# Kernel tuning notes

Hardware: AMD Instinct MI355X
Metric: run time of the kernel (lower is better)

The kernel has to match this reference:

```python
import jax, jax.numpy as jnp
import numpy as np

ALPHA = 1.8   # Levy stability index (undefined global in source; chosen heavy-tailed)
BETA = 0.0    # symmetric
SIGMA = 0.5
DEPTH = 25
DIM = 64
HID = 100
BATCH = 262144


def _levy_noise(u_raw, w_raw):
    """Chambers-Mallows-Stuck sampler for symmetric alpha-stable (beta=0).
    u_raw, w_raw ~ U(0,1); returns clipped noise, scale=0.1, clamp [-10,10]."""
    U = jnp.pi * (u_raw - 0.5)                       # U(-pi/2, pi/2)
    W = -jnp.log(jnp.clip(w_raw, 1e-12, 1.0))        # Exp(1)
    inv_a = 1.0 / ALPHA
    X = (jnp.sin(ALPHA * U) / jnp.cos(U) ** inv_a) * \
        (jnp.cos(U - ALPHA * U) / jnp.clip(W, 1e-12, None)) ** ((1.0 - ALPHA) * inv_a)
    return jnp.clip(0.1 * X, -10.0, 10.0)


def setup_inputs() -> dict:
    key = jax.random.key(0)
    ks = jax.random.split(key, 8)
    d, h = DIM, HID
    return {
        "x": jax.random.normal(ks[0], (BATCH, d), dtype=jnp.float32),
        "u_raw": jax.random.uniform(ks[1], (DEPTH, d), dtype=jnp.float32),
        "w_raw": jax.random.uniform(ks[2], (DEPTH, d), dtype=jnp.float32),
        "W_down": jax.random.normal(ks[3], (d, d), dtype=jnp.float32) / np.sqrt(d),
        "b_down": jnp.zeros((d,), jnp.float32),
        "W_drift": jax.random.normal(ks[4], (d, d), dtype=jnp.float32) / np.sqrt(d),
        "b_drift": jnp.zeros((d,), jnp.float32),
        "W1": jax.random.normal(ks[5], (d, h), dtype=jnp.float32) / np.sqrt(d),
        "b1": jnp.zeros((h,), jnp.float32),
        "W2": jax.random.normal(ks[6], (h, 1), dtype=jnp.float32) / np.sqrt(h),
        "b2": jnp.zeros((1,), jnp.float32),
    }


def reference(x, u_raw, w_raw, W_down, b_down, W_drift, b_drift, W1, b1, W2, b2):
    dt = 1.0 / DEPTH
    out = x @ W_down + b_down                                   # [B, d]
    # diffusion logit on the INITIAL state, held fixed through the loop
    logit = jax.nn.relu(out @ W1 + b1) @ W2 + b2                # [B, 1]
    scale = SIGMA * jax.nn.sigmoid(logit) * dt ** (1.0 / ALPHA)  # [B, 1]
    noise = _levy_noise(u_raw, w_raw)                           # [DEPTH, d]

    def step(out, n):
        drift = jax.nn.relu(out @ W_drift + b_drift) + out      # DriftNet: relu(lin)+x
        return out + drift * dt + scale * n, None

    out, _ = jax.lax.scan(step, out, noise)
    drift_out = jax.nn.relu(out @ W_drift + b_drift) + out
    return drift_out, out
```

## Files before the change

kernel.cpp:

```cpp
#include <hip/hip_runtime.h>
#include <hip/hip_bf16.h>

#define DEPTH 25
#define DIM   64
#define HID   100

typedef _Float16 f16x4 __attribute__((ext_vector_type(4)));
typedef float    f32x4 __attribute__((ext_vector_type(4)));
typedef float    f32x2 __attribute__((ext_vector_type(2)));

__global__ __launch_bounds__(64) void levy_noise_kernel(
    const float* __restrict__ u_raw, const float* __restrict__ w_raw,
    float* __restrict__ noise)
{
    const int idx = blockIdx.x * 64 + threadIdx.x;
    if (idx >= DEPTH * DIM) return;
    float u = u_raw[idx];
    float w = w_raw[idx];
    float U  = 3.14159265358979323846f * (u - 0.5f);
    float Wv = -logf(fminf(fmaxf(w, 1e-12f), 1.0f));
    float t1 = sinf(1.8f * U) / powf(cosf(U), 0.5555555555555556f);
    float ratio = cosf(0.8f * U) / fmaxf(Wv, 1e-12f);
    float X = t1 * powf(ratio, -0.4444444444444444f);
    noise[idx] = fminf(fmaxf(0.1f * X, -10.0f), 10.0f);
}

__global__ __launch_bounds__(256) void sdenet_fused(
    const float* __restrict__ x,      const float* __restrict__ noise_g,
    const float* __restrict__ W_down, const float* __restrict__ b_down,
    const float* __restrict__ W_drift,const float* __restrict__ b_drift,
    const float* __restrict__ W1,     const float* __restrict__ b1,
    const float* __restrict__ W2,     const float* __restrict__ b2,
    float* __restrict__ out, int batch)
{
    __shared__ float noise_lds[DEPTH * DIM];

    const int tid = threadIdx.x;
    {
        const float4* src = (const float4*)noise_g;
        float4* dst = (float4*)noise_lds;
        for (int idx = tid; idx < DEPTH * DIM / 4; idx += 256)
            dst[idx] = src[idx];
    }
    __syncthreads();

    const int wave = tid >> 6;
    const int lane = tid & 63;
    const int r    = lane & 15;
    const int g    = lane >> 4;
    const int row  = blockIdx.x * 64 + wave * 16 + r;
    const float dt = 0.04f;

    f16x4 bfrag[4];
    #pragma unroll
    for (int kt = 0; kt < 4; ++kt) {
        const float4 xv = *(const float4*)(x + row * DIM + kt * 16 + g * 4);
        f16x4 t;
        t[0] = (_Float16)xv.x; t[1] = (_Float16)xv.y;
        t[2] = (_Float16)xv.z; t[3] = (_Float16)xv.w;
        bfrag[kt] = t;
    }

    f32x2 out2[4][2];
    #pragma unroll
    for (int Mt = 0; Mt < 4; ++Mt) {
        f32x4 acc = *(const f32x4*)(b_down + Mt * 16 + g * 4);
        #pragma unroll
        for (int kt = 0; kt < 4; ++kt) {
            f16x4 a;
            #pragma unroll
            for (int i = 0; i < 4; ++i)
                a[i] = (_Float16)W_down[(kt * 16 + g * 4 + i) * DIM + Mt * 16 + r];
            acc = __builtin_amdgcn_mfma_f32_16x16x16f16(a, bfrag[kt], acc, 0, 0, 0);
        }
        out2[Mt][0][0] = acc[0]; out2[Mt][0][1] = acc[1];
        out2[Mt][1][0] = acc[2]; out2[Mt][1][1] = acc[3];
    }

    #pragma unroll
    for (int kt = 0; kt < 4; ++kt) {
        f16x4 t;
        t[0] = (_Float16)out2[kt][0][0]; t[1] = (_Float16)out2[kt][0][1];
        t[2] = (_Float16)out2[kt][1][0]; t[3] = (_Float16)out2[kt][1][1];
        bfrag[kt] = t;
    }

    float partial = 0.0f;
    #pragma unroll
    for (int Mt = 0; Mt < 7; ++Mt) {
        f32x4 acc;
        #pragma unroll
        for (int reg = 0; reg < 4; ++reg) {
            int n = Mt * 16 + g * 4 + reg;
            acc[reg] = (n < HID) ? b1[n] : 0.0f;
        }
        const int ncol = Mt * 16 + r;
        #pragma unroll
        for (int kt = 0; kt < 4; ++kt) {
            f16x4 a;
            #pragma unroll
            for (int i = 0; i < 4; ++i) {
                int k = kt * 16 + g * 4 + i;
                float v = (ncol < HID) ? W1[k * HID + ncol] : 0.0f;
                a[i] = (_Float16)v;
            }
            acc = __builtin_amdgcn_mfma_f32_16x16x16f16(a, bfrag[kt], acc, 0, 0, 0);
        }
        #pragma unroll
        for (int reg = 0; reg < 4; ++reg) {
            int n = Mt * 16 + g * 4 + reg;
            if (n < HID) partial += fmaxf(acc[reg], 0.0f) * W2[n];
        }
    }
    partial += __shfl_xor(partial, 16);
    partial += __shfl_xor(partial, 32);
    const float logit = partial + b2[0];
    const float scale = 0.5f * (1.0f / (1.0f + expf(-logit)))
                      * powf(0.04f, 1.0f / 1.8f);
    const f32x2 scale2 = { scale, scale };
    const f32x2 c104   = { 1.04f, 1.04f };
    const f32x2 zero2  = { 0.0f, 0.0f };

    f16x4 aWd[4][4];
    #pragma unroll
    for (int Mt = 0; Mt < 4; ++Mt)
        #pragma unroll
        for (int kt = 0; kt < 4; ++kt) {
            f16x4 a;
            #pragma unroll
            for (int i = 0; i < 4; ++i)
                a[i] = (_Float16)(dt * W_drift[(kt * 16 + g * 4 + i) * DIM + Mt * 16 + r]);
            aWd[Mt][kt] = a;
        }
    f32x4 biasd[4];
    #pragma unroll
    for (int Mt = 0; Mt < 4; ++Mt) {
        f32x4 b = *(const f32x4*)(b_drift + Mt * 16 + g * 4);
        biasd[Mt][0] = b[0] * dt; biasd[Mt][1] = b[1] * dt;
        biasd[Mt][2] = b[2] * dt; biasd[Mt][3] = b[3] * dt;
    }

    for (int t = 0; t < DEPTH; ++t) {
        f32x4 nz[4];
        #pragma unroll
        for (int Mt = 0; Mt < 4; ++Mt)
            nz[Mt] = *(const f32x4*)(noise_lds + t * DIM + Mt * 16 + g * 4);

        f32x4 acc[4];
        #pragma unroll
        for (int Mt = 0; Mt < 4; ++Mt) {
            acc[Mt] = biasd[Mt];
            #pragma unroll
            for (int kt = 0; kt < 4; ++kt)
                acc[Mt] = __builtin_amdgcn_mfma_f32_16x16x16f16(aWd[Mt][kt], bfrag[kt], acc[Mt], 0, 0, 0);
        }
        #pragma unroll
        for (int Mt = 0; Mt < 4; ++Mt) {
            #pragma unroll
            for (int h = 0; h < 2; ++h) {
                f32x2 a2 = { acc[Mt][2 * h], acc[Mt][2 * h + 1] };
                f32x2 n2 = { nz[Mt][2 * h],  nz[Mt][2 * h + 1] };
                f32x2 rel = __builtin_elementwise_max(a2, zero2);
                f32x2 tmp = __builtin_elementwise_fma(out2[Mt][h], c104, rel);
                out2[Mt][h] = __builtin_elementwise_fma(scale2, n2, tmp);
            }
        }
        #pragma unroll
        for (int kt = 0; kt < 4; ++kt) {
            f16x4 tt;
            tt[0] = (_Float16)out2[kt][0][0]; tt[1] = (_Float16)out2[kt][0][1];
            tt[2] = (_Float16)out2[kt][1][0]; tt[3] = (_Float16)out2[kt][1][1];
            bfrag[kt] = tt;
        }
    }

    const long long out2_off = (long long)batch * DIM;
    #pragma unroll
    for (int Mt = 0; Mt < 4; ++Mt) {
        f32x4 acc = biasd[Mt];
        #pragma unroll
        for (int kt = 0; kt < 4; ++kt)
            acc = __builtin_amdgcn_mfma_f32_16x16x16f16(aWd[Mt][kt], bfrag[kt], acc, 0, 0, 0);
        float o0 = out2[Mt][0][0], o1 = out2[Mt][0][1];
        float o2 = out2[Mt][1][0], o3 = out2[Mt][1][1];
        float4 dv, ov;
        dv.x = fmaf(fmaxf(acc[0], 0.0f), 25.0f, o0);
        dv.y = fmaf(fmaxf(acc[1], 0.0f), 25.0f, o1);
        dv.z = fmaf(fmaxf(acc[2], 0.0f), 25.0f, o2);
        dv.w = fmaf(fmaxf(acc[3], 0.0f), 25.0f, o3);
        ov.x = o0; ov.y = o1; ov.z = o2; ov.w = o3;
        *(float4*)(out + (long long)row * DIM + Mt * 16 + g * 4) = dv;
        *(float4*)(out + out2_off + (long long)row * DIM + Mt * 16 + g * 4) = ov;
    }
}

extern "C" void kernel_launch(void* const* d_in, const int* in_sizes, int n_in,
                              void* d_out, int out_size, void* d_ws, size_t ws_size,
                              hipStream_t stream) {
    const float* x       = (const float*)d_in[0];
    const float* u_raw   = (const float*)d_in[1];
    const float* w_raw   = (const float*)d_in[2];
    const float* W_down  = (const float*)d_in[3];
    const float* b_down  = (const float*)d_in[4];
    const float* W_drift = (const float*)d_in[5];
    const float* b_drift = (const float*)d_in[6];
    const float* W1      = (const float*)d_in[7];
    const float* b1      = (const float*)d_in[8];
    const float* W2      = (const float*)d_in[9];
    const float* b2      = (const float*)d_in[10];
    float* out   = (float*)d_out;
    float* noise = (float*)d_ws;

    const int batch = in_sizes[0] / DIM;
    const int blocks = batch / 64;

    levy_noise_kernel<<<DEPTH, 64, 0, stream>>>(u_raw, w_raw, noise);
    sdenet_fused<<<blocks, 256, 0, stream>>>(
        x, noise, W_down, b_down, W_drift, b_drift,
        W1, b1, W2, b2, out, batch);
}
```

Measured before the change: 280.0 us.

## Prepack weight fragments in prep kernel and process two row groups per wave

A single-block prep kernel now computes the Levy noise and also pre-converts W_down, dt-scaled W_drift and padded W1 into per-lane fp16 MFMA fragment order in device globals. The main kernel loads these with vector loads instead of doing strided scalar gathers and conversions. Each wave now handles two 16-row groups (128 rows per block), so the weight fragments are reused and two independent MFMA chains can interleave. Register pressure roughly doubles for state and accumulators, which may reduce occupancy, and the single-block prep kernel runs serially before the main kernel.

```diff
diff --git a/kernel.cpp b/kernel.cpp
--- a/kernel.cpp
+++ b/kernel.cpp
@@ -6,38 +6,74 @@
 #define HID   100
 
 typedef _Float16 f16x4 __attribute__((ext_vector_type(4)));
+typedef _Float16 f16x2 __attribute__((ext_vector_type(2)));
 typedef float    f32x4 __attribute__((ext_vector_type(4)));
 typedef float    f32x2 __attribute__((ext_vector_type(2)));
 
-__global__ __launch_bounds__(64) void levy_noise_kernel(
+static __device__ __forceinline__ f16x2 cvt_pk(float a, float b) {
+    return __builtin_bit_cast(f16x2, __builtin_amdgcn_cvt_pkrtz(a, b));
+}
+
+__device__ __align__(16) float    g_noise[DEPTH * DIM];
+__device__ __align__(16) float    g_b1p[112];
+__device__ __align__(16) float    g_W2p[112];
+__device__ __align__(16) _Float16 g_frWdown [64 * 64];
+__device__ __align__(16) _Float16 g_frWdrift[64 * 64];
+__device__ __align__(16) _Float16 g_frW1    [64 * 112];
+
+__global__ __launch_bounds__(256) void prep_kernel(
     const float* __restrict__ u_raw, const float* __restrict__ w_raw,
-    float* __restrict__ noise)
+    const float* __restrict__ W_down, const float* __restrict__ W_drift,
+    const float* __restrict__ W1,     const float* __restrict__ b1,
+    const float* __restrict__ W2)
 {
-    const int idx = blockIdx.x * 64 + threadIdx.x;
-    if (idx >= DEPTH * DIM) return;
-    float u = u_raw[idx];
-    float w = w_raw[idx];
-    float U  = 3.14159265358979323846f * (u - 0.5f);
-    float Wv = -logf(fminf(fmaxf(w, 1e-12f), 1.0f));
-    float t1 = sinf(1.8f * U) / powf(cosf(U), 0.5555555555555556f);
-    float ratio = cosf(0.8f * U) / fmaxf(Wv, 1e-12f);
-    float X = t1 * powf(ratio, -0.4444444444444444f);
-    noise[idx] = fminf(fmaxf(0.1f * X, -10.0f), 10.0f);
+    const int tid = threadIdx.x;
+
+    for (int idx = tid; idx < DEPTH * DIM; idx += 256) {
+        float u = u_raw[idx];
+        float w = w_raw[idx];
+        float U  = 3.14159265358979323846f * (u - 0.5f);
+        float Wv = -logf(fminf(fmaxf(w, 1e-12f), 1.0f));
+        float t1 = sinf(1.8f * U) / powf(cosf(U), 0.5555555555555556f);
+        float ratio = cosf(0.8f * U) / fmaxf(Wv, 1e-12f);
+        float X = t1 * powf(ratio, -0.4444444444444444f);
+        g_noise[idx] = fminf(fmaxf(0.1f * X, -10.0f), 10.0f);
+    }
+    if (tid < 112) {
+        g_b1p[tid] = (tid < HID) ? b1[tid] : 0.0f;
+        g_W2p[tid] = (tid < HID) ? W2[tid] : 0.0f;
+    }
+    if (tid < 64) {
+        const int l = tid, r = l & 15, g = l >> 4;
+        for (int Mt = 0; Mt < 4; ++Mt)
+            for (int kt = 0; kt < 4; ++kt)
+                for (int i = 0; i < 4; ++i) {
+                    int k = kt * 16 + g * 4 + i, col = Mt * 16 + r;
+                    g_frWdown [l * 64 + Mt * 16 + kt * 4 + i] = (_Float16)W_down[k * DIM + col];
+                    g_frWdrift[l * 64 + Mt * 16 + kt * 4 + i] = (_Float16)(0.04f * W_drift[k * DIM + col]);
+                }
+        for (int Mt = 0; Mt < 7; ++Mt) {
+            int ncol = Mt * 16 + r;
+            for (int kt = 0; kt < 4; ++kt)
+                for (int i = 0; i < 4; ++i) {
+                    int k = kt * 16 + g * 4 + i;
+                    g_frW1[l * 112 + Mt * 16 + kt * 4 + i] =
+                        (ncol < HID) ? (_Float16)W1[k * HID + ncol] : (_Float16)0.0f;
+                }
+        }
+    }
 }
 
 __global__ __launch_bounds__(256) void sdenet_fused(
-    const float* __restrict__ x,      const float* __restrict__ noise_g,
-    const float* __restrict__ W_down, const float* __restrict__ b_down,
-    const float* __restrict__ W_drift,const float* __restrict__ b_drift,
-    const float* __restrict__ W1,     const float* __restrict__ b1,
-    const float* __restrict__ W2,     const float* __restrict__ b2,
-    float* __restrict__ out, int batch)
+    const float* __restrict__ x,
+    const float* __restrict__ b_down, const float* __restrict__ b_drift,
+    const float* __restrict__ b2, float* __restrict__ out, int batch)
 {
     __shared__ float noise_lds[DEPTH * DIM];
 
     const int tid = threadIdx.x;
     {
-        const float4* src = (const float4*)noise_g;
+        const float4* src = (const float4*)g_noise;
         float4* dst = (float4*)noise_lds;
         for (int idx = tid; idx < DEPTH * DIM / 4; idx += 256)
             dst[idx] = src[idx];
@@ -48,97 +84,90 @@
     const int lane = tid & 63;
     const int r    = lane & 15;
     const int g    = lane >> 4;
-    const int row  = blockIdx.x * 64 + wave * 16 + r;
-    const float dt = 0.04f;
-
-    f16x4 bfrag[4];
+    const int row0 = blockIdx.x * 128 + wave * 32 + r;
+    const int row1 = row0 + 16;
+
+    f16x4 bfrag[2][4];
     #pragma unroll
     for (int kt = 0; kt < 4; ++kt) {
-        const float4 xv = *(const float4*)(x + row * DIM + kt * 16 + g * 4);
-        f16x4 t;
-        t[0] = (_Float16)xv.x; t[1] = (_Float16)xv.y;
-        t[2] = (_Float16)xv.z; t[3] = (_Float16)xv.w;
-        bfrag[kt] = t;
-    }
-
-    f32x2 out2[4][2];
+        const float4 xv0 = *(const float4*)(x + (long long)row0 * DIM + kt * 16 + g * 4);
+        const float4 xv1 = *(const float4*)(x + (long long)row1 * DIM + kt * 16 + g * 4);
+        f16x2 a0 = cvt_pk(xv0.x, xv0.y), a1 = cvt_pk(xv0.z, xv0.w);
+        f16x2 b0 = cvt_pk(xv1.x, xv1.y), b1v = cvt_pk(xv1.z, xv1.w);
+        bfrag[0][kt] = (f16x4){a0[0], a0[1], a1[0], a1[1]};
+        bfrag[1][kt] = (f16x4){b0[0], b0[1], b1v[0], b1v[1]};
+    }
+
+    f32x2 st[2][4][2];
     #pragma unroll
     for (int Mt = 0; Mt < 4; ++Mt) {
-        f32x4 acc = *(const f32x4*)(b_down + Mt * 16 + g * 4);
+        const f32x4 bdn = *(const f32x4*)(b_down + Mt * 16 + g * 4);
+        #pragma unroll
+        for (int gr = 0; gr < 2; ++gr) {
+            f32x4 acc = bdn;
+            #pragma unroll
+            for (int kt = 0; kt < 4; ++kt) {
+                const f16x4 a = *(const f16x4*)(g_frWdown + lane * 64 + Mt * 16 + kt * 4);
+                acc = __builtin_amdgcn_mfma_f32_16x16x16f16(a, bfrag[gr][kt], acc, 0, 0, 0);
+            }
+            st[gr][Mt][0] = (f32x2){acc[0], acc[1]};
+            st[gr][Mt][1] = (f32x2){acc[2], acc[3]};
+        }
+    }
+    #pragma unroll
+    for (int gr = 0; gr < 2; ++gr)
         #pragma unroll
         for (int kt = 0; kt < 4; ++kt) {
-            f16x4 a;
-            #pragma unroll
-            for (int i = 0; i < 4; ++i)
-                a[i] = (_Float16)W_down[(kt * 16 + g * 4 + i) * DIM + Mt * 16 + r];
-            acc = __builtin_amdgcn_mfma_f32_16x16x16f16(a, bfrag[kt], acc, 0, 0, 0);
-        }
-        out2[Mt][0][0] = acc[0]; out2[Mt][0][1] = acc[1];
-        out2[Mt][1][0] = acc[2]; out2[Mt][1][1] = acc[3];
-    }
-
-    #pragma unroll
-    for (int kt = 0; kt < 4; ++kt) {
-        f16x4 t;
-        t[0] = (_Float16)out2[kt][0][0]; t[1] = (_Float16)out2[kt][0][1];
-        t[2] = (_Float16)out2[kt][1][0]; t[3] = (_Float16)out2[kt][1][1];
-        bfrag[kt] = t;
-    }
-
-    float partial = 0.0f;
+            f16x2 lo = cvt_pk(st[gr][kt][0][0], st[gr][kt][0][1]);
+            f16x2 hi = cvt_pk(st[gr][kt][1][0], st[gr][kt][1][1]);
+            bfrag[gr][kt] = (f16x4){lo[0], lo[1], hi[0], hi[1]};
+        }
+
+    float partial[2] = {0.0f, 0.0f};
     #pragma unroll
     for (int Mt = 0; Mt < 7; ++Mt) {
-        f32x4 acc;
-        #pragma unroll
-        for (int reg = 0; reg < 4; ++reg) {
-            int n = Mt * 16 + g * 4 + reg;
-            acc[reg] = (n < HID) ? b1[n] : 0.0f;
-        }
-        const int ncol = Mt * 16 + r;
-        #pragma unroll
-        for (int kt = 0; kt < 4; ++kt) {
-            f16x4 a;
-            #pragma unroll
-            for (int i = 0; i < 4; ++i) {
-                int k = kt * 16 + g * 4 + i;
-                float v = (ncol < HID) ? W1[k * HID + ncol] : 0.0f;
-                a[i] = (_Float16)v;
-            }
-            acc = __builtin_amdgcn_mfma_f32_16x16x16f16(a, bfrag[kt], acc, 0, 0, 0);
-        }
-        #pragma unroll
-        for (int reg = 0; reg < 4; ++reg) {
-            int n = Mt * 16 + g * 4 + reg;
-            if (n < HID) partial += fmaxf(acc[reg], 0.0f) * W2[n];
-        }
-    }
-    partial += __shfl_xor(partial, 16);
-    partial += __shfl_xor(partial, 32);
-    const float logit = partial + b2[0];
-    const float scale = 0.5f * (1.0f / (1.0f + expf(-logit)))
+        const f32x4 binit = *(const f32x4*)(g_b1p + Mt * 16 + g * 4);
+        const f32x4 w2v   = *(const f32x4*)(g_W2p + Mt * 16 + g * 4);
+        #pragma unroll
+        for (int gr = 0; gr < 2; ++gr) {
+            f32x4 acc = binit;
+            #pragma unroll
+            for (int kt = 0; kt < 4; ++kt) {
+                const f16x4 a = *(const f16x4*)(g_frW1 + lane * 112 + Mt * 16 + kt * 4);
+                acc = __builtin_amdgcn_mfma_f32_16x16x16f16(a, bfrag[gr][kt], acc, 0, 0, 0);
+            }
+            #pragma unroll
+            for (int reg = 0; reg < 4; ++reg)
+                partial[gr] += fmaxf(acc[reg], 0.0f) * w2v[reg];
+        }
+    }
+    f32x2 scl[2];
+    #pragma unroll
+    for (int gr = 0; gr < 2; ++gr) {
+        float p = partial[gr];
+        p += __shfl_xor(p, 16);
+        p += __shfl_xor(p, 32);
+        const float logit = p + b2[0];
+        const float s = 0.5f * (1.0f / (1.0f + expf(-logit)))
                       * powf(0.04f, 1.0f / 1.8f);
-    const f32x2 scale2 = { scale, scale };
-    const f32x2 c104   = { 1.04f, 1.04f };
-    const f32x2 zero2  = { 0.0f, 0.0f };
+        scl[gr] = (f32x2){s, s};
+    }
 
     f16x4 aWd[4][4];
     #pragma unroll
     for (int Mt = 0; Mt < 4; ++Mt)
         #pragma unroll
-        for (int kt = 0; kt < 4; ++kt) {
-            f16x4 a;
-            #pragma unroll
-            for (int i = 0; i < 4; ++i)
-                a[i] = (_Float16)(dt * W_drift[(kt * 16 + g * 4 + i) * DIM + Mt * 16 + r]);
-            aWd[Mt][kt] = a;
-        }
+        for (int kt = 0; kt < 4; ++kt)
+            aWd[Mt][kt] = *(const f16x4*)(g_frWdrift + lane * 64 + Mt * 16 + kt * 4);
     f32x4 biasd[4];
     #pragma unroll
     for (int Mt = 0; Mt < 4; ++Mt) {
         f32x4 b = *(const f32x4*)(b_drift + Mt * 16 + g * 4);
-        biasd[Mt][0] = b[0] * dt; biasd[Mt][1] = b[1] * dt;
-        biasd[Mt][2] = b[2] * dt; biasd[Mt][3] = b[3] * dt;
-    }
+        biasd[Mt] = (f32x4){b[0] * 0.04f, b[1] * 0.04f, b[2] * 0.04f, b[3] * 0.04f};
+    }
+
+    const f32x2 c104 = {1.04f, 1.04f};
+    const f32x2 zero2 = {0.0f, 0.0f};
 
     for (int t = 0; t < DEPTH; ++t) {
         f32x4 nz[4];
@@ -146,51 +175,60 @@
         for (int Mt = 0; Mt < 4; ++Mt)
             nz[Mt] = *(const f32x4*)(noise_lds + t * DIM + Mt * 16 + g * 4);
 
-        f32x4 acc[4];
+        f32x4 acc[2][4];
+        #pragma unroll
+        for (int gr = 0; gr < 2; ++gr)
+            #pragma unroll
+            for (int Mt = 0; Mt < 4; ++Mt) {
+                acc[gr][Mt] = biasd[Mt];
+                #pragma unroll
+                for (int kt = 0; kt < 4; ++kt)
+                    acc[gr][Mt] = __builtin_amdgcn_mfma_f32_16x16x16f16(
+                        aWd[Mt][kt], bfrag[gr][kt], acc[gr][Mt], 0, 0, 0);
+            }
+        #pragma unroll
+        for (int gr = 0; gr < 2; ++gr) {
+            #pragma unroll
+            for (int Mt = 0; Mt < 4; ++Mt) {
+                #pragma unroll
+                for (int h = 0; h < 2; ++h) {
+                    f32x2 a2 = {acc[gr][Mt][2 * h], acc[gr][Mt][2 * h + 1]};
+                    f32x2 n2 = {nz[Mt][2 * h], nz[Mt][2 * h + 1]};
+                    f32x2 rel = __builtin_elementwise_max(a2, zero2);
+                    f32x2 tmp = __builtin_elementwise_fma(st[gr][Mt][h], c104, rel);
+                    st[gr][Mt][h] = __builtin_elementwise_fma(scl[gr], n2, tmp);
+                }
+            }
+            #pragma unroll
+            for (int kt = 0; kt < 4; ++kt) {
+                f16x2 lo = cvt_pk(st[gr][kt][0][0], st[gr][kt][0][1]);
+                f16x2 hi = cvt_pk(st[gr][kt][1][0], st[gr][kt][1][1]);
+                bfrag[gr][kt] = (f16x4){lo[0], lo[1], hi[0], hi[1]};
+            }
+        }
+    }
+
+    const long long out2_off = (long long)batch * DIM;
+    #pragma unroll
+    for (int gr = 0; gr < 2; ++gr) {
+        const long long rowg = (gr == 0) ? row0 : row1;
         #pragma unroll
         for (int Mt = 0; Mt < 4; ++Mt) {
-            acc[Mt] = biasd[Mt];
+            f32x4 acc = biasd[Mt];
             #pragma unroll
             for (int kt = 0; kt < 4; ++kt)
-                acc[Mt] = __builtin_amdgcn_mfma_f32_16x16x16f16(aWd[Mt][kt], bfrag[kt], acc[Mt], 0, 0, 0);
-        }
-        #pragma unroll
-        for (int Mt = 0; Mt < 4; ++Mt) {
-            #pragma unroll
-            for (int h = 0; h < 2; ++h) {
-                f32x2 a2 = { acc[Mt][2 * h], acc[Mt][2 * h + 1] };
-                f32x2 n2 = { nz[Mt][2 * h],  nz[Mt][2 * h + 1] };
-                f32x2 rel = __builtin_elementwise_max(a2, zero2);
-                f32x2 tmp = __builtin_elementwise_fma(out2[Mt][h], c104, rel);
-                out2[Mt][h] = __builtin_elementwise_fma(scale2, n2, tmp);
-            }
-        }
-        #pragma unroll
-        for (int kt = 0; kt < 4; ++kt) {
-            f16x4 tt;
-            tt[0] = (_Float16)out2[kt][0][0]; tt[1] = (_Float16)out2[kt][0][1];
-            tt[2] = (_Float16)out2[kt][1][0]; tt[3] = (_Float16)out2[kt][1][1];
-            bfrag[kt] = tt;
-        }
-    }
-
-    const long long out2_off = (long long)batch * DIM;
-    #pragma unroll
-    for (int Mt = 0; Mt < 4; ++Mt) {
-        f32x4 acc = biasd[Mt];
-        #pragma unroll
-        for (int kt = 0; kt < 4; ++kt)
-            acc = __builtin_amdgcn_mfma_f32_16x16x16f16(aWd[Mt][kt], bfrag[kt], acc, 0, 0, 0);
-        float o0 = out2[Mt][0][0], o1 = out2[Mt][0][1];
-        float o2 = out2[Mt][1][0], o3 = out2[Mt][1][1];
-        float4 dv, ov;
-        dv.x = fmaf(fmaxf(acc[0], 0.0f), 25.0f, o0);
-        dv.y = fmaf(fmaxf(acc[1], 0.0f), 25.0f, o1);
-        dv.z = fmaf(fmaxf(acc[2], 0.0f), 25.0f, o2);
-        dv.w = fmaf(fmaxf(acc[3], 0.0f), 25.0f, o3);
-        ov.x = o0; ov.y = o1; ov.z = o2; ov.w = o3;
-        *(float4*)(out + (long long)row * DIM + Mt * 16 + g * 4) = dv;
-        *(float4*)(out + out2_off + (long long)row * DIM + Mt * 16 + g * 4) = ov;
+                acc = __builtin_amdgcn_mfma_f32_16x16x16f16(aWd[Mt][kt], bfrag[gr][kt], acc, 0, 0, 0);
+            float o0 = st[gr][Mt][0][0], o1 = st[gr][Mt][0][1];
+            float o2 = st[gr][Mt][1][0], o3 = st[gr][Mt][1][1];
+            float4 dv, ov;
+            dv.x = fmaf(fmaxf(acc[0], 0.0f), 25.0f, o0);
+            dv.y = fmaf(fmaxf(acc[1], 0.0f), 25.0f, o1);
+            dv.z = fmaf(fmaxf(acc[2], 0.0f), 25.0f, o2);
+            dv.w = fmaf(fmaxf(acc[3], 0.0f), 25.0f, o3);
+            ov.x = o0; ov.y = o1; ov.z = o2; ov.w = o3;
+            *(float4*)(out + rowg * DIM + Mt * 16 + g * 4) = dv;
+            *(float4*)(out + out2_off + rowg * DIM + Mt * 16 + g * 4) = ov;
+        }
     }
 }
 
@@ -208,14 +246,11 @@
     const float* b1      = (const float*)d_in[8];
     const float* W2      = (const float*)d_in[9];
     const float* b2      = (const float*)d_in[10];
-    float* out   = (float*)d_out;
-    float* noise = (float*)d_ws;
+    float* out = (float*)d_out;
 
     const int batch = in_sizes[0] / DIM;
-    const int blocks = batch / 64;
-
-    levy_noise_kernel<<<DEPTH, 64, 0, stream>>>(u_raw, w_raw, noise);
-    sdenet_fused<<<blocks, 256, 0, stream>>>(
-        x, noise, W_down, b_down, W_drift, b_drift,
-        W1, b1, W2, b2, out, batch);
-}
+    const int blocks = batch / 128;
+
+    prep_kernel<<<1, 256, 0, stream>>>(u_raw, w_raw, W_down, W_drift, W1, b1, W2);
+    sdenet_fused<<<blocks, 256, 0, stream>>>(x, b_down, b_drift, b2, out, batch);
+}
```

After: 295.9 us. 1.06x slower.
